# Optimization experiments

Hardware: AMD Instinct MI355X
Metric: run time of the kernel (lower is better)

## Reference

```python
import jax, jax.numpy as jnp
import numpy as np

NSAMPLE = 16
GROUPS = 8  # 128 // 16 per nn.GroupNorm(C//16, C)
EPS = 1e-5


def _conv1d(w, b, x):
    # 1x1 Conv1d: w [O,C], x [B,C,N]
    return jnp.einsum('oc,bcn->bon', w, x) + b[None, :, None]


def _conv2d(w, b, x):
    # 1x1 Conv2d: w [O,C], x [B,C,N,K]
    return jnp.einsum('oc,bcnk->bonk', w, x) + b[None, :, None, None]


def _gn(x, g, b):
    # GroupNorm over (C//G, N, K) per (batch, group), as torch GroupNorm on NCHW
    B, C, N, K = x.shape
    xg = x.reshape(B, GROUPS, C // GROUPS, N, K)
    mu = xg.mean(axis=(2, 3, 4), keepdims=True)
    var = ((xg - mu) ** 2).mean(axis=(2, 3, 4), keepdims=True)
    xn = ((xg - mu) * jax.lax.rsqrt(var + EPS)).reshape(B, C, N, K)
    return xn * g[None, :, None, None] + b[None, :, None, None]


def _lrelu(x):
    return jnp.where(x >= 0, x, 0.1 * x)


def _knn_idx(xyz1, xyz2, k):
    # squared pairwise distances (monotone in torch.norm -> same top-k indices)
    s1 = jnp.sum(xyz1 * xyz1, axis=1)  # [B,N1]
    s2 = jnp.sum(xyz2 * xyz2, axis=1)  # [B,N2]
    d2 = s1[:, :, None] + s2[:, None, :] - 2.0 * jnp.einsum('bcn,bcm->bnm', xyz1, xyz2)
    return jax.lax.top_k(-d2, k)[1]  # [B,N1,K] nearest neighbors


def _group(points, idx):
    # points [B,C,N2], idx [B,N1,K] -> [B,C,N1,K]  (pointnet2 grouping_operation)
    return jax.vmap(lambda p, i: p[:, i])(points, idx)


def _cross(xyz1, xyz2, p1, p2, pos_w, pos_b, gn_g, gn_b, mlp_params):
    idx = _knn_idx(xyz1, xyz2, NSAMPLE)
    neighbor_xyz = _group(xyz2, idx)                      # [B,3,N1,K]
    direction = neighbor_xyz - xyz1[:, :, :, None]
    gp2 = _group(p2, idx)                                 # [B,C,N1,K]
    pos_feat = _conv2d(pos_w, pos_b, direction)
    new_points = _lrelu(_gn(gp2 + p1[:, :, :, None] + pos_feat, gn_g, gn_b))
    for (w, b, g, bb) in mlp_params:
        new_points = _lrelu(_gn(_conv2d(w, b, new_points), g, bb))
    return jnp.max(new_points, axis=3)                    # max-pool over K


def setup_inputs() -> dict:
    key = jax.random.key(0)
    ks = jax.random.split(key, 40)
    B, N, CIN, C = 2, 4096, 64, 128
    f32 = jnp.float32

    def w(k, o, i):
        return jax.random.normal(k, (o, i), f32) * 0.05

    inp = {
        'pc1': jax.random.normal(ks[0], (B, 3, N), f32),
        'pc2': jax.random.normal(ks[1], (B, 3, N), f32),
        'feat1': jax.random.normal(ks[2], (B, CIN, N), f32),
        'feat2': jax.random.normal(ks[3], (B, CIN, N), f32),
        't11_w': w(ks[4], C, CIN), 't11_b': jnp.zeros((C,), f32),
        't22_w': w(ks[5], C, CIN), 't22_b': jnp.zeros((C,), f32),
        'pos1_w': w(ks[6], C, 3), 'pos1_b': jnp.zeros((C,), f32),
        'gn1_g': jnp.ones((C,), f32), 'gn1_b': jnp.zeros((C,), f32),
        'm1a_w': w(ks[7], C, C), 'm1a_b': jnp.zeros((C,), f32),
        'm1a_g': jnp.ones((C,), f32), 'm1a_beta': jnp.zeros((C,), f32),
        'm1b_w': w(ks[8], C, C), 'm1b_b': jnp.zeros((C,), f32),
        'm1b_g': jnp.ones((C,), f32), 'm1b_beta': jnp.zeros((C,), f32),
        't1_w': w(ks[9], C, C), 't1_b': jnp.zeros((C,), f32),
        't2_w': w(ks[10], C, C), 't2_b': jnp.zeros((C,), f32),
        'pos2_w': w(ks[11], C, 3), 'pos2_b': jnp.zeros((C,), f32),
        'gn2_g': jnp.ones((C,), f32), 'gn2_b': jnp.zeros((C,), f32),
        'm2a_w': w(ks[12], C, C), 'm2a_b': jnp.zeros((C,), f32),
        'm2a_g': jnp.ones((C,), f32), 'm2a_beta': jnp.zeros((C,), f32),
    }
    return inp


def reference(pc1, pc2, feat1, feat2,
              t11_w, t11_b, t22_w, t22_b,
              pos1_w, pos1_b, gn1_g, gn1_b,
              m1a_w, m1a_b, m1a_g, m1a_beta,
              m1b_w, m1b_b, m1b_g, m1b_beta,
              t1_w, t1_b, t2_w, t2_b,
              pos2_w, pos2_b, gn2_g, gn2_b,
              m2a_w, m2a_b, m2a_g, m2a_beta):
    mlp1 = [(m1a_w, m1a_b, m1a_g, m1a_beta), (m1b_w, m1b_b, m1b_g, m1b_beta)]
    mlp2 = [(m2a_w, m2a_b, m2a_g, m2a_beta)]
    f1 = _conv1d(t11_w, t11_b, feat1)
    f2 = _conv1d(t22_w, t22_b, feat2)
    g1 = _conv1d(t11_w, t11_b, feat2)
    g2 = _conv1d(t22_w, t22_b, feat1)
    feat1_new = _conv1d(t1_w, t1_b, _cross(pc1, pc2, f1, f2, pos1_w, pos1_b, gn1_g, gn1_b, mlp1))
    feat2_new = _conv1d(t2_w, t2_b, _cross(pc2, pc1, g1, g2, pos1_w, pos1_b, gn1_g, gn1_b, mlp1))
    feat1_final = _cross(pc1, pc2, feat1_new, feat2_new, pos2_w, pos2_b, gn2_g, gn2_b, mlp2)
    return (feat1_new, feat2_new, feat1_final)
```

## Files before the change

### kernel.cpp

```cpp
#include <hip/hip_runtime.h>
#include <hip/hip_bf16.h>

#define NPTS 4096
#define CC   128
#define KNN  16
#define CNT_PER_GROUP 1048576.0f
#define STAT_STRIDE 1024

typedef __attribute__((ext_vector_type(8))) short bf16x8;
typedef __attribute__((ext_vector_type(8))) unsigned short u16x8;
typedef __attribute__((ext_vector_type(4))) float f32x4;
typedef unsigned short ushort_t;

static __device__ __forceinline__ ushort_t f2bf(float f) {
    __hip_bfloat16 h = __float2bfloat16(f);
    ushort_t u; __builtin_memcpy(&u, &h, 2);
    return u;
}
static __device__ __forceinline__ float bf2f(ushort_t u) {
    unsigned v = (unsigned)u << 16;
    float f; __builtin_memcpy(&f, &v, 4);
    return f;
}

__global__ void prep_kernel(const float* __restrict__ t11_w, const float* __restrict__ t22_w,
                            const float* __restrict__ t1_w,  const float* __restrict__ t2_w,
                            const float* __restrict__ m1a_w, const float* __restrict__ m1b_w,
                            const float* __restrict__ m2a_w,
                            float* __restrict__ wTt11, float* __restrict__ wTt22,
                            float* __restrict__ wTt1,  float* __restrict__ wTt2,
                            ushort_t* __restrict__ W2m1a, ushort_t* __restrict__ W2m1b,
                            ushort_t* __restrict__ W2m2a, float* __restrict__ stats) {
    int y = blockIdx.y;
    int idx = blockIdx.x * 256 + threadIdx.x;
    if (y == 7) {
        if (idx < 8 * STAT_STRIDE) stats[idx] = 0.0f;
        return;
    }
    if (y < 4) {
        const float* in; float* outp; int Cdim;
        switch (y) {
            case 0: in = t11_w; outp = wTt11; Cdim = 64; break;
            case 1: in = t22_w; outp = wTt22; Cdim = 64; break;
            case 2: in = t1_w;  outp = wTt1;  Cdim = CC; break;
            default: in = t2_w; outp = wTt2;  Cdim = CC; break;
        }
        if (idx < CC * Cdim) {
            int o = idx / Cdim, c = idx % Cdim;
            outp[c * CC + o] = in[idx];
        }
        return;
    }
    const float* in = y == 4 ? m1a_w : y == 5 ? m1b_w : m2a_w;
    ushort_t* outp  = y == 4 ? W2m1a : y == 5 ? W2m1b : W2m2a;
    if (idx < 16384) {
        int j = idx & 7, lane = (idx >> 3) & 63, coT = (idx >> 9) & 7, kb = idx >> 12;
        int k  = kb * 32 + (lane >> 4) * 8 + j;
        int co = coT * 16 + (lane & 15);
        outp[idx] = f2bf(in[co * CC + k]);
    }
}

__global__ __launch_bounds__(256) void conv64_kernel(
        const float* __restrict__ feat1, const float* __restrict__ feat2,
        const float* __restrict__ wTt11, const float* __restrict__ wTt22,
        const float* __restrict__ b11, const float* __restrict__ b22,
        float* __restrict__ f1, float* __restrict__ f2,
        float* __restrict__ g1, float* __restrict__ g2) {
    __shared__ float xs[64][68];
    int y = blockIdx.y;
    const float* x  = (y == 0 || y == 3) ? feat1 : feat2;
    const float* wT = (y == 0 || y == 2) ? wTt11 : wTt22;
    const float* bias = (y == 0 || y == 2) ? b11 : b22;
    float* outp = y == 0 ? f1 : y == 1 ? f2 : y == 2 ? g1 : g2;
    int tid = threadIdx.x;
    int n0 = blockIdx.x * 64;
    int b = n0 >> 12, nloc = n0 & 4095;
    const float* xb = x + (size_t)b * 64 * NPTS + nloc;
    #pragma unroll
    for (int i = 0; i < 16; ++i) {
        int e = tid + 256 * i;
        int ci = e >> 6, nn = e & 63;
        xs[ci][nn] = xb[(size_t)ci * NPTS + nn];
    }
    __syncthreads();
    int co = (tid & 31) * 4;
    int r0 = (tid >> 5) * 8;
    float acc[4][8];
    float4 bv = *(const float4*)&bias[co];
    #pragma unroll
    for (int j = 0; j < 8; ++j) { acc[0][j] = bv.x; acc[1][j] = bv.y; acc[2][j] = bv.z; acc[3][j] = bv.w; }
    for (int ci = 0; ci < 64; ++ci) {
        float4 wv = *(const float4*)&wT[(size_t)ci * CC + co];
        #pragma unroll
        for (int j = 0; j < 8; ++j) {
            float xv = xs[ci][r0 + j];
            acc[0][j] += wv.x * xv;
            acc[1][j] += wv.y * xv;
            acc[2][j] += wv.z * xv;
            acc[3][j] += wv.w * xv;
        }
    }
    #pragma unroll
    for (int j = 0; j < 8; ++j) {
        *(float4*)&outp[(size_t)(n0 + r0 + j) * CC + co] =
            make_float4(acc[0][j], acc[1][j], acc[2][j], acc[3][j]);
    }
}

static __device__ __forceinline__ unsigned long long sxor64(unsigned long long v, int m) {
    unsigned lo = (unsigned)__shfl_xor((int)(unsigned)v, m);
    unsigned hi = (unsigned)__shfl_xor((int)(v >> 32), m);
    return ((unsigned long long)hi << 32) | lo;
}

__global__ __launch_bounds__(512) void knn_kernel(
        const float* __restrict__ pc1, const float* __restrict__ pc2,
        int* __restrict__ idx12, int* __restrict__ idx21) {
#pragma clang fp contract(off)
    __shared__ float4 pk[NPTS];
    __shared__ unsigned long long lst[8][4][64];
    int dir = blockIdx.y;
    const float* qs = dir ? pc2 : pc1;
    const float* cs = dir ? pc1 : pc2;
    int* outIdx = dir ? idx21 : idx12;
    int tid = threadIdx.x, lane = tid & 63, wv = tid >> 6;
    int qbase = blockIdx.x * 32;
    int b = qbase >> 12;
    const float* cb = cs + (size_t)b * 3 * NPTS;
    for (int i = tid; i < NPTS; i += 512) {
        float x = cb[i], y = cb[NPTS + i], z = cb[2 * NPTS + i];
        pk[i] = make_float4(x, y, z, x * x + y * y + z * z);
    }
    __syncthreads();
    const float* qb = qs + (size_t)b * 3 * NPTS;
    int q0 = qbase + wv * 4;
    float qx[4], qy[4], qz[4], s1[4], dmin[4], T[4];
    #pragma unroll
    for (int t = 0; t < 4; ++t) {
        int n = (q0 + t) & 4095;
        qx[t] = qb[n]; qy[t] = qb[NPTS + n]; qz[t] = qb[2 * NPTS + n];
        s1[t] = qx[t] * qx[t] + qy[t] * qy[t] + qz[t] * qz[t];
        dmin[t] = 1e30f;
    }
    for (int j = 0; j < 64; ++j) {
        float4 P = pk[j * 64 + lane];
        #pragma unroll
        for (int t = 0; t < 4; ++t) {
            float dt = __builtin_fmaf(P.z, qz[t], __builtin_fmaf(P.y, qy[t], P.x * qx[t]));
            float d2 = (s1[t] + P.w) - 2.0f * dt;
            dmin[t] = fminf(dmin[t], d2);
        }
    }
    #pragma unroll
    for (int t = 0; t < 4; ++t) {
        float sv = dmin[t];
        for (int k = 2; k <= 64; k <<= 1)
            for (int j = k >> 1; j > 0; j >>= 1) {
                float o = __shfl_xor(sv, j);
                bool tmin = (((lane & k) == 0) == ((lane & j) == 0));
                sv = tmin ? fminf(sv, o) : fmaxf(sv, o);
            }
        T[t] = __shfl(sv, 15);
    }
    int base[4] = {0, 0, 0, 0};
    for (int j = 0; j < 64; ++j) {
        float4 P = pk[j * 64 + lane];
        int m = j * 64 + lane;
        #pragma unroll
        for (int t = 0; t < 4; ++t) {
            float dt = __builtin_fmaf(P.z, qz[t], __builtin_fmaf(P.y, qy[t], P.x * qx[t]));
            float d2 = (s1[t] + P.w) - 2.0f * dt;
            bool p = (d2 <= T[t]);
            unsigned long long mk = __ballot(p);
            if (p) {
                int pos = base[t] + (int)__popcll(mk & ((1ULL << lane) - 1ULL));
                unsigned u = __float_as_uint(d2);
                u ^= (unsigned)(((int)u >> 31) | 0x80000000);
                unsigned long long key = ((unsigned long long)u << 32) | (unsigned)m;
                if (pos < 64) lst[wv][t][pos] = key;
            }
            base[t] += (int)__popcll(mk);
        }
    }
    #pragma unroll
    for (int t = 0; t < 4; ++t) {
        int nT = base[t] < 64 ? base[t] : 64;
        unsigned long long key = (lane < nT) ? lst[wv][t][lane] : ~0ULL;
        for (int k = 2; k <= 64; k <<= 1)
            for (int j = k >> 1; j > 0; j >>= 1) {
                unsigned long long o = sxor64(key, j);
                bool tmin = (((lane & k) == 0) == ((lane & j) == 0));
                unsigned long long mn = key < o ? key : o;
                unsigned long long mx = key < o ? o : key;
                key = tmin ? mn : mx;
            }
        if (lane < KNN) outIdx[(size_t)(q0 + t) * KNN + lane] = (int)(unsigned)(key & 0xFFFFFFFFULL);
    }
}

__global__ void h0_kernel(const float* __restrict__ p1f, const float* __restrict__ p2f,
                          const float* __restrict__ pcA, const float* __restrict__ pcB,
                          const int* __restrict__ idx,
                          const float* __restrict__ pos_w, const float* __restrict__ pos_b,
                          ushort_t* __restrict__ buf, float* __restrict__ stats_out) {
    __shared__ float redS[128], redQ[128];
    int p = blockIdx.x;
    int b = p >> 12, n = p & 4095;
    int c = threadIdx.x;
    float pw0 = pos_w[c * 3], pw1 = pos_w[c * 3 + 1], pw2 = pos_w[c * 3 + 2];
    float pb = pos_b[c];
    float p1v = p1f[(size_t)p * CC + c];
    const float* pa = pcA + (size_t)b * 3 * NPTS;
    const float* pc = pcB + (size_t)b * 3 * NPTS;
    float qx = pa[n], qy = pa[NPTS + n], qz = pa[2 * NPTS + n];
    float S = 0.f, Q = 0.f;
    for (int k = 0; k < KNN; ++k) {
        int m = idx[(size_t)p * KNN + k];
        float dx = pc[m] - qx;
        float dy = pc[NPTS + m] - qy;
        float dz = pc[2 * NPTS + m] - qz;
        float pos = pw0 * dx + pw1 * dy + pw2 * dz + pb;
        float v = p2f[((size_t)b * NPTS + m) * CC + c] + p1v + pos;
        buf[((size_t)p * KNN + k) * CC + c] = f2bf(v);
        S += v; Q += v * v;
    }
    redS[c] = S; redQ[c] = Q;
    __syncthreads();
    if (c < 8) {
        float SS = 0.f, QQ = 0.f;
        for (int i = 0; i < 16; ++i) { SS += redS[c * 16 + i]; QQ += redQ[c * 16 + i]; }
        int s = blockIdx.x & 31;
        atomicAdd(&stats_out[s * 32 + (b * 8 + c) * 2],     SS);
        atomicAdd(&stats_out[s * 32 + (b * 8 + c) * 2 + 1], QQ);
    }
}

__global__ __launch_bounds__(256) void convgn_kernel(
        const ushort_t* __restrict__ xbuf, const float* __restrict__ stats_in,
        const float* __restrict__ gam, const float* __restrict__ bet,
        const ushort_t* __restrict__ W2, const float* __restrict__ bias,
        ushort_t* __restrict__ ybuf, float* __restrict__ stats_out) {
    __shared__ ushort_t xt[64 * 136];
    __shared__ float sc[CC], sh[CC];
    __shared__ float redS[4][8], redQ[4][8];
    int tid = threadIdx.x;
    int s0 = blockIdx.x * 64;
    int b = s0 >> 16;
    if (tid < CC) {
        int g = tid >> 4;
        float S = 0.f, Q = 0.f;
        for (int s = 0; s < 32; ++s) {
            S += stats_in[s * 32 + (b * 8 + g) * 2];
            Q += stats_in[s * 32 + (b * 8 + g) * 2 + 1];
        }
        float mu = S / CNT_PER_GROUP;
        float var = Q / CNT_PER_GROUP - mu * mu;
        float rs = rsqrtf(var + 1e-5f);
        float scale = gam[tid] * rs;
        sc[tid] = scale;
        sh[tid] = bet[tid] - mu * scale;
    }
    __syncthreads();
    #pragma unroll
    for (int j = 0; j < 4; ++j) {
        int idx = tid + 256 * j;
        int row = idx >> 4, c8 = (idx & 15) * 8;
        u16x8 vin = *(const u16x8*)&xbuf[(size_t)(s0 + row) * CC + c8];
        u16x8 vo;
        #pragma unroll
        for (int e = 0; e < 8; ++e) {
            float v = bf2f(vin[e]) * sc[c8 + e] + sh[c8 + e];
            v = v >= 0.f ? v : 0.1f * v;
            vo[e] = f2bf(v);
        }
        *(u16x8*)&xt[row * 136 + c8] = vo;
    }
    __syncthreads();
    int lane = tid & 63, wv = tid >> 6;
    int r0 = wv * 16;
    int quad = lane >> 4;
    f32x4 acc[8];
    #pragma unroll
    for (int t = 0; t < 8; ++t) acc[t] = (f32x4){0.f, 0.f, 0.f, 0.f};
    int aoff = (r0 + (lane & 15)) * 136 + quad * 8;
    #pragma unroll
    for (int kb = 0; kb < 4; ++kb) {
        bf16x8 a = *(const bf16x8*)&xt[aoff + kb * 32];
        const ushort_t* wb = W2 + (size_t)kb * 4096 + lane * 8;
        #pragma unroll
        for (int t = 0; t < 8; ++t) {
            bf16x8 bf = *(const bf16x8*)&wb[t * 512];
            acc[t] = __builtin_amdgcn_mfma_f32_16x16x32_bf16(a, bf, acc[t], 0, 0, 0);
        }
    }
    #pragma unroll
    for (int t = 0; t < 8; ++t) {
        int co = t * 16 + (lane & 15);
        float bv = bias[co];
        float S = 0.f, Q = 0.f;
        #pragma unroll
        for (int reg = 0; reg < 4; ++reg) {
            int row = s0 + r0 + quad * 4 + reg;
            float y = acc[t][reg] + bv;
            ybuf[(size_t)row * CC + co] = f2bf(y);
            S += y; Q += y * y;
        }
        #pragma unroll
        for (int off = 1; off < 64; off <<= 1) {
            S += __shfl_xor(S, off);
            Q += __shfl_xor(Q, off);
        }
        if (lane == 0) { redS[wv][t] = S; redQ[wv][t] = Q; }
    }
    __syncthreads();
    if (tid < 8) {
        float S = redS[0][tid] + redS[1][tid] + redS[2][tid] + redS[3][tid];
        float Q = redQ[0][tid] + redQ[1][tid] + redQ[2][tid] + redQ[3][tid];
        int s = blockIdx.x & 31;
        atomicAdd(&stats_out[s * 32 + (b * 8 + tid) * 2],     S);
        atomicAdd(&stats_out[s * 32 + (b * 8 + tid) * 2 + 1], Q);
    }
}

__global__ __launch_bounds__(256) void maxpool_kernel(
        const ushort_t* __restrict__ ybuf, const float* __restrict__ stats,
        const float* __restrict__ gam, const float* __restrict__ bet,
        float* __restrict__ outb) {
    int p0 = blockIdx.x * 16;
    int b = p0 >> 12, n0 = p0 & 4095;
    int tid = threadIdx.x;
    int c = tid & 127, half = tid >> 7;
    int g = c >> 4;
    float S = 0.f, Q = 0.f;
    for (int s = 0; s < 32; ++s) {
        S += stats[s * 32 + (b * 8 + g) * 2];
        Q += stats[s * 32 + (b * 8 + g) * 2 + 1];
    }
    float mu = S / CNT_PER_GROUP;
    float var = Q / CNT_PER_GROUP - mu * mu;
    float rs = rsqrtf(var + 1e-5f);
    float scale = gam[c] * rs;
    float shift = bet[c] - mu * scale;
    float* orow = outb + ((size_t)b * CC + c) * NPTS + n0 + half * 8;
    #pragma unroll
    for (int j = 0; j < 8; ++j) {
        int nl = half * 8 + j;
        float mx = -INFINITY;
        for (int k = 0; k < KNN; ++k) {
            float v = bf2f(ybuf[((size_t)(p0 + nl) * KNN + k) * CC + c]) * scale + shift;
            v = v >= 0.f ? v : 0.1f * v;
            mx = fmaxf(mx, v);
        }
        orow[j] = mx;
    }
}

__global__ __launch_bounds__(256) void maxconv_kernel(
        const ushort_t* __restrict__ ybuf, const float* __restrict__ stats,
        const float* __restrict__ gam, const float* __restrict__ bet,
        const float* __restrict__ wT, const float* __restrict__ bias,
        float* __restrict__ outf, float* __restrict__ outb) {
    __shared__ float mxs[16][CC + 4];
    int p0 = blockIdx.x * 16;
    int b = p0 >> 12, n0 = p0 & 4095;
    int tid = threadIdx.x;
    int c = tid & 127, half = tid >> 7;
    int g = c >> 4;
    float S = 0.f, Q = 0.f;
    for (int s = 0; s < 32; ++s) {
        S += stats[s * 32 + (b * 8 + g) * 2];
        Q += stats[s * 32 + (b * 8 + g) * 2 + 1];
    }
    float mu = S / CNT_PER_GROUP;
    float var = Q / CNT_PER_GROUP - mu * mu;
    float rs = rsqrtf(var + 1e-5f);
    float scale = gam[c] * rs;
    float shift = bet[c] - mu * scale;
    #pragma unroll
    for (int j = 0; j < 8; ++j) {
        int nl = half * 8 + j;
        float mx = -INFINITY;
        for (int k = 0; k < KNN; ++k) {
            float v = bf2f(ybuf[((size_t)(p0 + nl) * KNN + k) * CC + c]) * scale + shift;
            v = v >= 0.f ? v : 0.1f * v;
            mx = fmaxf(mx, v);
        }
        mxs[nl][c] = mx;
    }
    __syncthreads();
    float acc[8];
    float bv = bias[c];
    #pragma unroll
    for (int j = 0; j < 8; ++j) acc[j] = bv;
    for (int ci = 0; ci < CC; ++ci) {
        float wv = wT[(size_t)ci * CC + c];
        #pragma unroll
        for (int j = 0; j < 8; ++j)
            acc[j] += wv * mxs[half * 8 + j][ci];
    }
    #pragma unroll
    for (int j = 0; j < 8; ++j)
        outf[(size_t)(p0 + half * 8 + j) * CC + c] = acc[j];
    float* orow = outb + ((size_t)b * CC + c) * NPTS + n0 + half * 8;
    #pragma unroll
    for (int j = 0; j < 8; ++j) orow[j] = acc[j];
}

extern "C" void kernel_launch(void* const* d_in, const int* in_sizes, int n_in,
                              void* d_out, int out_size, void* d_ws, size_t ws_size,
                              hipStream_t stream) {
    (void)in_sizes; (void)n_in; (void)out_size; (void)ws_size;
    const float* pc1    = (const float*)d_in[0];
    const float* pc2    = (const float*)d_in[1];
    const float* feat1  = (const float*)d_in[2];
    const float* feat2  = (const float*)d_in[3];
    const float* t11_w  = (const float*)d_in[4];
    const float* t11_b  = (const float*)d_in[5];
    const float* t22_w  = (const float*)d_in[6];
    const float* t22_b  = (const float*)d_in[7];
    const float* pos1_w = (const float*)d_in[8];
    const float* pos1_b = (const float*)d_in[9];
    const float* gn1_g  = (const float*)d_in[10];
    const float* gn1_b  = (const float*)d_in[11];
    const float* m1a_w  = (const float*)d_in[12];
    const float* m1a_b  = (const float*)d_in[13];
    const float* m1a_g  = (const float*)d_in[14];
    const float* m1a_be = (const float*)d_in[15];
    const float* m1b_w  = (const float*)d_in[16];
    const float* m1b_b  = (const float*)d_in[17];
    const float* m1b_g  = (const float*)d_in[18];
    const float* m1b_be = (const float*)d_in[19];
    const float* t1_w   = (const float*)d_in[20];
    const float* t1_b   = (const float*)d_in[21];
    const float* t2_w   = (const float*)d_in[22];
    const float* t2_b   = (const float*)d_in[23];
    const float* pos2_w = (const float*)d_in[24];
    const float* pos2_b = (const float*)d_in[25];
    const float* gn2_g  = (const float*)d_in[26];
    const float* gn2_b  = (const float*)d_in[27];
    const float* m2a_w  = (const float*)d_in[28];
    const float* m2a_b  = (const float*)d_in[29];
    const float* m2a_g  = (const float*)d_in[30];
    const float* m2a_be = (const float*)d_in[31];

    float* out = (float*)d_out;
    const size_t PN = 2 * NPTS;
    const size_t PT = PN * CC;
    float* ws   = (float*)d_ws;
    float* f1   = ws;
    float* f2   = f1 + PT;
    float* g1   = f2 + PT;
    float* g2   = g1 + PT;
    float* f1n  = g2 + PT;
    float* f2n  = f1n + PT;
    int*   idx12 = (int*)(f2n + PT);
    int*   idx21 = idx12 + PN * KNN;
    float* stats = (float*)(idx21 + PN * KNN);
    float* wTt11 = stats + 8 * STAT_STRIDE;
    float* wTt22 = wTt11 + 64 * CC;
    float* wTt1  = wTt22 + 64 * CC;
    float* wTt2  = wTt1 + CC * CC;
    ushort_t* W2m1a = (ushort_t*)(wTt2 + CC * CC);
    ushort_t* W2m1b = W2m1a + 16384;
    ushort_t* W2m2a = W2m1b + 16384;
    ushort_t* bufX  = W2m2a + 16384;
    ushort_t* bufY  = bufX + (size_t)PN * KNN * CC;

    prep_kernel<<<dim3(64, 8), 256, 0, stream>>>(
        t11_w, t22_w, t1_w, t2_w, m1a_w, m1b_w, m2a_w,
        wTt11, wTt22, wTt1, wTt2, W2m1a, W2m1b, W2m2a, stats);

    conv64_kernel<<<dim3(PN / 64, 4), 256, 0, stream>>>(
        feat1, feat2, wTt11, wTt22, t11_b, t22_b, f1, f2, g1, g2);
    knn_kernel<<<dim3(PN / 32, 2), 512, 0, stream>>>(pc1, pc2, idx12, idx21);

    float* st0 = stats;
    h0_kernel<<<PN, 128, 0, stream>>>(f1, f2, pc1, pc2, idx12, pos1_w, pos1_b, bufX, st0 + 0 * STAT_STRIDE);
    convgn_kernel<<<2048, 256, 0, stream>>>(bufX, st0 + 0 * STAT_STRIDE, gn1_g, gn1_b, W2m1a, m1a_b, bufY, st0 + 1 * STAT_STRIDE);
    convgn_kernel<<<2048, 256, 0, stream>>>(bufY, st0 + 1 * STAT_STRIDE, m1a_g, m1a_be, W2m1b, m1b_b, bufX, st0 + 2 * STAT_STRIDE);
    maxconv_kernel<<<PN / 16, 256, 0, stream>>>(bufX, st0 + 2 * STAT_STRIDE, m1b_g, m1b_be, wTt1, t1_b, f1n, out);

    h0_kernel<<<PN, 128, 0, stream>>>(g1, g2, pc2, pc1, idx21, pos1_w, pos1_b, bufX, st0 + 3 * STAT_STRIDE);
    convgn_kernel<<<2048, 256, 0, stream>>>(bufX, st0 + 3 * STAT_STRIDE, gn1_g, gn1_b, W2m1a, m1a_b, bufY, st0 + 4 * STAT_STRIDE);
    convgn_kernel<<<2048, 256, 0, stream>>>(bufY, st0 + 4 * STAT_STRIDE, m1a_g, m1a_be, W2m1b, m1b_b, bufX, st0 + 5 * STAT_STRIDE);
    maxconv_kernel<<<PN / 16, 256, 0, stream>>>(bufX, st0 + 5 * STAT_STRIDE, m1b_g, m1b_be, wTt2, t2_b, f2n, out + PT);

    h0_kernel<<<PN, 128, 0, stream>>>(f1n, f2n, pc1, pc2, idx12, pos2_w, pos2_b, bufX, st0 + 6 * STAT_STRIDE);
    convgn_kernel<<<2048, 256, 0, stream>>>(bufX, st0 + 6 * STAT_STRIDE, gn2_g, gn2_b, W2m2a, m2a_b, bufY, st0 + 7 * STAT_STRIDE);
    maxpool_kernel<<<PN / 16, 256, 0, stream>>>(bufY, st0 + 7 * STAT_STRIDE, m2a_g, m2a_be, out + 2 * PT);
}
```

Before: 397.9 us.

## Batch both cross passes per launch, stage convgn stores via LDS, atomic knn compaction

The two first-stage cross computations are independent, so they now run together in one grid with blockIdx.y selecting the pass. Each of h0, convgn and maxconv therefore launches once instead of twice, which doubles the per-launch parallelism and removes serialized launch tails; it needs separate X/Y buffers per pass. The convgn output is staged through shared memory and written with vectorized 16-byte stores instead of scattered 2-byte stores. The knn candidate compaction switches from ballot/popcount to per-wave LDS atomics, with capacity reduced to 63, which changes candidate ordering and may add atomic contention.

```diff
diff --git a/kernel.cpp b/kernel.cpp
--- a/kernel.cpp
+++ b/kernel.cpp
@@ -119,7 +119,8 @@
         int* __restrict__ idx12, int* __restrict__ idx21) {
 #pragma clang fp contract(off)
     __shared__ float4 pk[NPTS];
-    __shared__ unsigned long long lst[8][4][64];
+    __shared__ unsigned long long lst[8][4][63];
+    __shared__ int cnt[8][4];
     int dir = blockIdx.y;
     const float* qs = dir ? pc2 : pc1;
     const float* cs = dir ? pc1 : pc2;
@@ -163,7 +164,7 @@
             }
         T[t] = __shfl(sv, 15);
     }
-    int base[4] = {0, 0, 0, 0};
+    if (lane < 4) cnt[wv][lane] = 0;
     for (int j = 0; j < 64; ++j) {
         float4 P = pk[j * 64 + lane];
         int m = j * 64 + lane;
@@ -171,21 +172,17 @@
         for (int t = 0; t < 4; ++t) {
             float dt = __builtin_fmaf(P.z, qz[t], __builtin_fmaf(P.y, qy[t], P.x * qx[t]));
             float d2 = (s1[t] + P.w) - 2.0f * dt;
-            bool p = (d2 <= T[t]);
-            unsigned long long mk = __ballot(p);
-            if (p) {
-                int pos = base[t] + (int)__popcll(mk & ((1ULL << lane) - 1ULL));
+            if (d2 <= T[t]) {
                 unsigned u = __float_as_uint(d2);
                 u ^= (unsigned)(((int)u >> 31) | 0x80000000);
-                unsigned long long key = ((unsigned long long)u << 32) | (unsigned)m;
-                if (pos < 64) lst[wv][t][pos] = key;
+                int pos = atomicAdd(&cnt[wv][t], 1);
+                if (pos < 63) lst[wv][t][pos] = ((unsigned long long)u << 32) | (unsigned)m;
             }
-            base[t] += (int)__popcll(mk);
         }
     }
     #pragma unroll
     for (int t = 0; t < 4; ++t) {
-        int nT = base[t] < 64 ? base[t] : 64;
+        int nT = cnt[wv][t]; if (nT > 63) nT = 63;
         unsigned long long key = (lane < nT) ? lst[wv][t][lane] : ~0ULL;
         for (int k = 2; k <= 64; k <<= 1)
             for (int j = k >> 1; j > 0; j >>= 1) {
@@ -199,12 +196,22 @@
     }
 }
 
-__global__ void h0_kernel(const float* __restrict__ p1f, const float* __restrict__ p2f,
-                          const float* __restrict__ pcA, const float* __restrict__ pcB,
-                          const int* __restrict__ idx,
+__global__ void h0_kernel(const float* p1f_1, const float* p2f_1,
+                          const float* p1f_2, const float* p2f_2,
+                          const float* __restrict__ pc1, const float* __restrict__ pc2,
+                          const int* idx_1, const int* idx_2,
                           const float* __restrict__ pos_w, const float* __restrict__ pos_b,
-                          ushort_t* __restrict__ buf, float* __restrict__ stats_out) {
+                          ushort_t* buf_1, ushort_t* buf_2,
+                          float* stats_1, float* stats_2) {
     __shared__ float redS[128], redQ[128];
+    int y = blockIdx.y;
+    const float* p1f = y ? p1f_2 : p1f_1;
+    const float* p2f = y ? p2f_2 : p2f_1;
+    const float* pcA = y ? pc2 : pc1;
+    const float* pcB = y ? pc1 : pc2;
+    const int* idx = y ? idx_2 : idx_1;
+    ushort_t* buf = y ? buf_2 : buf_1;
+    float* stats_out = y ? stats_2 : stats_1;
     int p = blockIdx.x;
     int b = p >> 12, n = p & 4095;
     int c = threadIdx.x;
@@ -237,13 +244,20 @@
 }
 
 __global__ __launch_bounds__(256) void convgn_kernel(
-        const ushort_t* __restrict__ xbuf, const float* __restrict__ stats_in,
+        const ushort_t* xbuf_1, const ushort_t* xbuf_2,
+        const float* stats_in_1, const float* stats_in_2,
         const float* __restrict__ gam, const float* __restrict__ bet,
         const ushort_t* __restrict__ W2, const float* __restrict__ bias,
-        ushort_t* __restrict__ ybuf, float* __restrict__ stats_out) {
+        ushort_t* ybuf_1, ushort_t* ybuf_2,
+        float* stats_out_1, float* stats_out_2) {
     __shared__ ushort_t xt[64 * 136];
     __shared__ float sc[CC], sh[CC];
     __shared__ float redS[4][8], redQ[4][8];
+    int y = blockIdx.y;
+    const ushort_t* xbuf = y ? xbuf_2 : xbuf_1;
+    const float* stats_in = y ? stats_in_2 : stats_in_1;
+    ushort_t* ybuf = y ? ybuf_2 : ybuf_1;
+    float* stats_out = y ? stats_out_2 : stats_out_1;
     int tid = threadIdx.x;
     int s0 = blockIdx.x * 64;
     int b = s0 >> 16;
@@ -301,10 +315,10 @@
         float S = 0.f, Q = 0.f;
         #pragma unroll
         for (int reg = 0; reg < 4; ++reg) {
-            int row = s0 + r0 + quad * 4 + reg;
-            float y = acc[t][reg] + bv;
-            ybuf[(size_t)row * CC + co] = f2bf(y);
-            S += y; Q += y * y;
+            int rl = r0 + quad * 4 + reg;
+            float yv = acc[t][reg] + bv;
+            xt[rl * 136 + co] = f2bf(yv);
+            S += yv; Q += yv * yv;
         }
         #pragma unroll
         for (int off = 1; off < 64; off <<= 1) {
@@ -312,6 +326,14 @@
             Q += __shfl_xor(Q, off);
         }
         if (lane == 0) { redS[wv][t] = S; redQ[wv][t] = Q; }
+    }
+    #pragma unroll
+    for (int i = 0; i < 4; ++i) {
+        int chunk = i * 64 + lane;
+        int rl = r0 + (chunk >> 4);
+        int c8 = (chunk & 15) * 8;
+        u16x8 v = *(const u16x8*)&xt[rl * 136 + c8];
+        *(u16x8*)&ybuf[(size_t)(s0 + rl) * CC + c8] = v;
     }
     __syncthreads();
     if (tid < 8) {
@@ -357,11 +379,21 @@
 }
 
 __global__ __launch_bounds__(256) void maxconv_kernel(
-        const ushort_t* __restrict__ ybuf, const float* __restrict__ stats,
+        const ushort_t* ybuf_1, const ushort_t* ybuf_2,
+        const float* stats_1, const float* stats_2,
         const float* __restrict__ gam, const float* __restrict__ bet,
-        const float* __restrict__ wT, const float* __restrict__ bias,
-        float* __restrict__ outf, float* __restrict__ outb) {
+        const float* wT_1, const float* wT_2,
+        const float* bias_1, const float* bias_2,
+        float* outf_1, float* outf_2,
+        float* __restrict__ outb) {
     __shared__ float mxs[16][CC + 4];
+    int y = blockIdx.y;
+    const ushort_t* ybuf = y ? ybuf_2 : ybuf_1;
+    const float* stats = y ? stats_2 : stats_1;
+    const float* wT = y ? wT_2 : wT_1;
+    const float* bias = y ? bias_2 : bias_1;
+    float* outf = y ? outf_2 : outf_1;
+    float* ob = outb + (size_t)y * 2 * NPTS * CC;
     int p0 = blockIdx.x * 16;
     int b = p0 >> 12, n0 = p0 & 4095;
     int tid = threadIdx.x;
@@ -402,7 +434,7 @@
     #pragma unroll
     for (int j = 0; j < 8; ++j)
         outf[(size_t)(p0 + half * 8 + j) * CC + c] = acc[j];
-    float* orow = outb + ((size_t)b * CC + c) * NPTS + n0 + half * 8;
+    float* orow = ob + ((size_t)b * CC + c) * NPTS + n0 + half * 8;
     #pragma unroll
     for (int j = 0; j < 8; ++j) orow[j] = acc[j];
 }
@@ -464,8 +496,10 @@
     ushort_t* W2m1a = (ushort_t*)(wTt2 + CC * CC);
     ushort_t* W2m1b = W2m1a + 16384;
     ushort_t* W2m2a = W2m1b + 16384;
-    ushort_t* bufX  = W2m2a + 16384;
-    ushort_t* bufY  = bufX + (size_t)PN * KNN * CC;
+    ushort_t* bufX1 = W2m2a + 16384;
+    ushort_t* bufY1 = bufX1 + (size_t)PN * KNN * CC;
+    ushort_t* bufX2 = bufY1 + (size_t)PN * KNN * CC;
+    ushort_t* bufY2 = bufX2 + (size_t)PN * KNN * CC;
 
     prep_kernel<<<dim3(64, 8), 256, 0, stream>>>(
         t11_w, t22_w, t1_w, t2_w, m1a_w, m1b_w, m2a_w,
@@ -476,17 +510,28 @@
     knn_kernel<<<dim3(PN / 32, 2), 512, 0, stream>>>(pc1, pc2, idx12, idx21);
 
     float* st0 = stats;
-    h0_kernel<<<PN, 128, 0, stream>>>(f1, f2, pc1, pc2, idx12, pos1_w, pos1_b, bufX, st0 + 0 * STAT_STRIDE);
-    convgn_kernel<<<2048, 256, 0, stream>>>(bufX, st0 + 0 * STAT_STRIDE, gn1_g, gn1_b, W2m1a, m1a_b, bufY, st0 + 1 * STAT_STRIDE);
-    convgn_kernel<<<2048, 256, 0, stream>>>(bufY, st0 + 1 * STAT_STRIDE, m1a_g, m1a_be, W2m1b, m1b_b, bufX, st0 + 2 * STAT_STRIDE);
-    maxconv_kernel<<<PN / 16, 256, 0, stream>>>(bufX, st0 + 2 * STAT_STRIDE, m1b_g, m1b_be, wTt1, t1_b, f1n, out);
-
-    h0_kernel<<<PN, 128, 0, stream>>>(g1, g2, pc2, pc1, idx21, pos1_w, pos1_b, bufX, st0 + 3 * STAT_STRIDE);
-    convgn_kernel<<<2048, 256, 0, stream>>>(bufX, st0 + 3 * STAT_STRIDE, gn1_g, gn1_b, W2m1a, m1a_b, bufY, st0 + 4 * STAT_STRIDE);
-    convgn_kernel<<<2048, 256, 0, stream>>>(bufY, st0 + 4 * STAT_STRIDE, m1a_g, m1a_be, W2m1b, m1b_b, bufX, st0 + 5 * STAT_STRIDE);
-    maxconv_kernel<<<PN / 16, 256, 0, stream>>>(bufX, st0 + 5 * STAT_STRIDE, m1b_g, m1b_be, wTt2, t2_b, f2n, out + PT);
-
-    h0_kernel<<<PN, 128, 0, stream>>>(f1n, f2n, pc1, pc2, idx12, pos2_w, pos2_b, bufX, st0 + 6 * STAT_STRIDE);
-    convgn_kernel<<<2048, 256, 0, stream>>>(bufX, st0 + 6 * STAT_STRIDE, gn2_g, gn2_b, W2m2a, m2a_b, bufY, st0 + 7 * STAT_STRIDE);
-    maxpool_kernel<<<PN / 16, 256, 0, stream>>>(bufY, st0 + 7 * STAT_STRIDE, m2a_g, m2a_be, out + 2 * PT);
-}
+    h0_kernel<<<dim3(PN, 2), 128, 0, stream>>>(
+        f1, f2, g1, g2, pc1, pc2, idx12, idx21, pos1_w, pos1_b,
+        bufX1, bufX2, st0 + 0 * STAT_STRIDE, st0 + 3 * STAT_STRIDE);
+    convgn_kernel<<<dim3(2048, 2), 256, 0, stream>>>(
+        bufX1, bufX2, st0 + 0 * STAT_STRIDE, st0 + 3 * STAT_STRIDE,
+        gn1_g, gn1_b, W2m1a, m1a_b,
+        bufY1, bufY2, st0 + 1 * STAT_STRIDE, st0 + 4 * STAT_STRIDE);
+    convgn_kernel<<<dim3(2048, 2), 256, 0, stream>>>(
+        bufY1, bufY2, st0 + 1 * STAT_STRIDE, st0 + 4 * STAT_STRIDE,
+        m1a_g, m1a_be, W2m1b, m1b_b,
+        bufX1, bufX2, st0 + 2 * STAT_STRIDE, st0 + 5 * STAT_STRIDE);
+    maxconv_kernel<<<dim3(PN / 16, 2), 256, 0, stream>>>(
+        bufX1, bufX2, st0 + 2 * STAT_STRIDE, st0 + 5 * STAT_STRIDE,
+        m1b_g, m1b_be, wTt1, wTt2, t1_b, t2_b, f1n, f2n, out);
+
+    h0_kernel<<<dim3(PN, 1), 128, 0, stream>>>(
+        f1n, f2n, f1n, f2n, pc1, pc2, idx12, idx12, pos2_w, pos2_b,
+        bufX1, bufX1, st0 + 6 * STAT_STRIDE, st0 + 6 * STAT_STRIDE);
+    convgn_kernel<<<dim3(2048, 1), 256, 0, stream>>>(
+        bufX1, bufX1, st0 + 6 * STAT_STRIDE, st0 + 6 * STAT_STRIDE,
+        gn2_g, gn2_b, W2m2a, m2a_b,
+        bufY1, bufY1, st0 + 7 * STAT_STRIDE, st0 + 7 * STAT_STRIDE);
+    maxpool_kernel<<<PN / 16, 256, 0, stream>>>(
+        bufY1, st0 + 7 * STAT_STRIDE, m2a_g, m2a_be, out + 2 * PT);
+}
```

New measurement: 375.7 us. 5.6% less time.
